# Kernel tuning notes

Hardware: AMD Instinct MI355X
Metric: run time of the kernel (lower is better)

The kernel has to match this reference:

```python
import jax, jax.numpy as jnp
import numpy as np

DIM = 1024
MAXLEN = 2048
EPS = 1e-6


def rms_norm(x, w):
    rms = jnp.sqrt(jnp.mean(x * x, axis=-1, keepdims=True) + EPS)
    return x / rms * w


def setup_inputs() -> dict:
    key = jax.random.key(0)
    ks = jax.random.split(key, 12)
    d = DIM
    s = 0.02
    inp = {
        "x": jax.random.normal(ks[0], (8, 2048, d), dtype=jnp.float32),
        "attn_norm_w": jnp.ones((d,), jnp.float32),
        "mlp_norm_w": jnp.ones((d,), jnp.float32),
        "wq": jax.random.normal(ks[1], (d, d), jnp.float32) * s,
        "bq": jnp.zeros((d,), jnp.float32),
        "wk": jax.random.normal(ks[2], (d, d), jnp.float32) * s,
        "bk": jnp.zeros((d,), jnp.float32),
        "wv": jax.random.normal(ks[3], (d, d), jnp.float32) * s,
        "bv": jnp.zeros((d,), jnp.float32),
        "wo": jax.random.normal(ks[4], (d, d), jnp.float32) * s,
        "bo": jnp.zeros((d,), jnp.float32),
        "w1": jax.random.normal(ks[5], (d, 4 * d), jnp.float32) * s,
        "b1": jnp.zeros((4 * d,), jnp.float32),
        "w2": jax.random.normal(ks[6], (4 * d, d), jnp.float32) * s,
        "b2": jnp.zeros((d,), jnp.float32),
    }
    return inp


def reference(x, attn_norm_w, mlp_norm_w, wq, bq, wk, bk, wv, bv, wo, bo, w1, b1, w2, b2):
    b, t, d = x.shape
    xn = rms_norm(x, attn_norm_w)
    q = xn @ wq + bq
    k = xn @ wk + bk
    v = xn @ wv + bv
    # single-head attention over full dim, scaled by sqrt(d)
    scores = jnp.einsum("btd,bsd->bts", q, k) / jnp.sqrt(jnp.asarray(d, x.dtype))
    causal = jnp.tril(jnp.ones((t, t), dtype=bool))
    scores = jnp.where(causal, scores, jnp.asarray(-1e9, x.dtype))
    probs = jax.nn.softmax(scores, axis=-1)
    attn = jnp.einsum("bts,bsd->btd", probs, v)
    x = x + attn @ wo + bo
    h = rms_norm(x, mlp_norm_w)
    x = x + jax.nn.gelu(h @ w1 + b1, approximate=False) @ w2 + b2
    return x
```

## Files before the change

kernel.cpp:

```cpp
#include <hip/hip_runtime.h>
#include <hip/hip_bf16.h>

typedef __bf16 bf16;
typedef __bf16 bf16x8 __attribute__((ext_vector_type(8)));
typedef __bf16 bf16x4 __attribute__((ext_vector_type(4)));
typedef float  f32x4  __attribute__((ext_vector_type(4)));

#define DIM   1024
#define SEQ   2048
#define BATCH 8
#define NROWS (BATCH * SEQ)
#define HID   4096

__device__ __forceinline__ void async_ld16(const bf16* g, bf16* l) {
    __builtin_amdgcn_global_load_lds(
        (__attribute__((address_space(1))) void*)(g),
        (__attribute__((address_space(3))) void*)(l),
        16, 0, 0);
}

__device__ __forceinline__ f32x4 mfma16(bf16x8 a, bf16x8 b, f32x4 c) {
    return __builtin_amdgcn_mfma_f32_16x16x32_bf16(a, b, c, 0, 0, 0);
}

template<int OUTF32, int BIASMODE, int RESID, int GELU, int SCORE, int PV>
__global__ __launch_bounds__(512, 2) void gemm256_kernel(
    const bf16* __restrict__ A, size_t aB,
    const bf16* __restrict__ B, size_t bB,
    void* __restrict__ Cv, size_t cB,
    const float* __restrict__ bias,
    const float* __restrict__ resid,
    int M, int N, int K, float scale)
{
    __shared__ alignas(16) bf16 LA[2 * 2 * 8192];
    __shared__ alignas(16) bf16 LB[2 * 2 * 8192];

    const int gx = gridDim.x;
    int lin = blockIdx.y * gx + blockIdx.x;
    {
        const int nwg = gx * gridDim.y;
        const int q = nwg >> 3, r = nwg & 7;
        const int xcd = lin & 7, o = lin >> 3;
        lin = (xcd < r ? xcd * (q + 1) : r * (q + 1) + (xcd - r) * q) + o;
    }
    const int m0 = (lin / gx) * 256;
    const int n0 = (lin % gx) * 256;
    if (SCORE && n0 >= m0 + 256) return;

    const int z = blockIdx.z;
    A += (size_t)z * aB;
    B += (size_t)z * bB;

    const int t    = threadIdx.x;
    const int lane = t & 63;
    const int wave = t >> 6;
    const int wr   = wave >> 2;
    const int wc   = wave & 3;

    const int kEnd = PV ? (m0 + 256) : K;
    const int NT   = kEnd >> 6;

    const int srow = t >> 3;
    const int sd   = ((t & 7) ^ (srow & 7)) * 8;
    const bf16* gA = A + (size_t)(m0 + srow) * (size_t)K + sd;
    const bf16* gB = B + (size_t)(n0 + srow) * (size_t)K + sd;
    bf16* const lA = LA + wave * 512;
    bf16* const lB = LB + wave * 512;
    const size_t rowblk = (size_t)64 * (size_t)K;

#define STG_A(db, hf, T) do {                                               \
    const bf16* g_ = gA + (size_t)((hf) * 2) * rowblk + (size_t)(T) * 64;   \
    async_ld16(g_,          lA + ((db) * 2 + (hf)) * 8192);                 \
    async_ld16(g_ + rowblk, lA + ((db) * 2 + (hf)) * 8192 + 4096);          \
} while (0)
#define STG_B(db, hf, T) do {                                               \
    const bf16* g_ = gB + (size_t)((hf) * 2) * rowblk + (size_t)(T) * 64;   \
    async_ld16(g_,          lB + ((db) * 2 + (hf)) * 8192);                 \
    async_ld16(g_ + rowblk, lB + ((db) * 2 + (hf)) * 8192 + 4096);          \
} while (0)

    const int fr    = lane & 15;
    const int fg    = lane >> 4;
    const int pc0   = ((fg)     ^ (fr & 7)) * 8;
    const int pc1   = ((4 + fg) ^ (fr & 7)) * 8;
    const int raOff = (wr * 64 + fr) * 64;
    const int rbOff = (wc * 32 + fr) * 64;

    f32x4  acc[2][2][4][2] = {};
    bf16x8 af[4][2];
    bf16x8 bg[2][2][2];

#define LDF_A(db, hf) do { _Pragma("unroll")                                  \
    for (int mi_ = 0; mi_ < 4; ++mi_) {                                       \
        const bf16* p_ = LA + ((db) * 2 + (hf)) * 8192 + raOff + mi_ * 1024;  \
        af[mi_][0] = *(const bf16x8*)(p_ + pc0);                              \
        af[mi_][1] = *(const bf16x8*)(p_ + pc1); } } while (0)
#define LDF_B(db, hf) do { _Pragma("unroll")                                  \
    for (int ni_ = 0; ni_ < 2; ++ni_) {                                       \
        const bf16* p_ = LB + ((db) * 2 + (hf)) * 8192 + rbOff + ni_ * 1024;  \
        bg[hf][ni_][0] = *(const bf16x8*)(p_ + pc0);                          \
        bg[hf][ni_][1] = *(const bf16x8*)(p_ + pc1); } } while (0)
#define MFMAQ(qm, qn) do {                                                    \
    __builtin_amdgcn_s_setprio(1);                                            \
    _Pragma("unroll") for (int mi_ = 0; mi_ < 4; ++mi_)                       \
    _Pragma("unroll") for (int ni_ = 0; ni_ < 2; ++ni_) {                     \
        acc[qm][qn][mi_][ni_] = mfma16(af[mi_][0], bg[qn][ni_][0], acc[qm][qn][mi_][ni_]); \
        acc[qm][qn][mi_][ni_] = mfma16(af[mi_][1], bg[qn][ni_][1], acc[qm][qn][mi_][ni_]); } \
    __builtin_amdgcn_s_setprio(0);                                            \
} while (0)
#define LGKM0 do { asm volatile("s_waitcnt lgkmcnt(0)" ::: "memory");         \
                   __builtin_amdgcn_sched_barrier(0); } while (0)
#define VM6   asm volatile("s_waitcnt vmcnt(6)" ::: "memory")
#define VM8   asm volatile("s_waitcnt vmcnt(8)" ::: "memory")
#define BAR   __builtin_amdgcn_s_barrier()

    STG_A(0, 0, 0); STG_B(0, 0, 0); STG_B(0, 1, 0); STG_A(0, 1, 0);
    STG_A(1, 0, 1); STG_B(1, 0, 1); STG_B(1, 1, 1); STG_A(1, 1, 1);
    VM8;
    BAR;
    LDF_A(0, 0); LDF_B(0, 0); LDF_B(0, 1);

    for (int kt = 0; kt < NT; kt += 2) {
        const int Tp2 = (kt + 2 < NT) ? kt + 2 : NT - 1;
        const int Tp3 = (kt + 3 < NT) ? kt + 3 : NT - 1;

        LGKM0;
        STG_A(0, 0, Tp2); STG_B(0, 0, Tp2);
        MFMAQ(0, 0); MFMAQ(0, 1);
        LDF_A(0, 1);
        VM6; BAR;

        LGKM0;
        STG_B(0, 1, Tp2); STG_A(0, 1, Tp2);
        MFMAQ(1, 0);
        LDF_B(1, 0);
        MFMAQ(1, 1);
        LDF_B(1, 1);
        LDF_A(1, 0);
        VM8; BAR;

        LGKM0;
        STG_A(1, 0, Tp3); STG_B(1, 0, Tp3);
        MFMAQ(0, 0); MFMAQ(0, 1);
        LDF_A(1, 1);
        VM6; BAR;

        LGKM0;
        STG_B(1, 1, Tp3); STG_A(1, 1, Tp3);
        MFMAQ(1, 0);
        LDF_B(0, 0);
        MFMAQ(1, 1);
        LDF_B(0, 1);
        LDF_A(0, 0);
        VM8; BAR;
    }

    const int col  = lane & 15;
    const int row4 = (lane >> 4) * 4;
    const size_t cOff = (size_t)z * cB;
    #pragma unroll
    for (int qm = 0; qm < 2; ++qm)
    #pragma unroll
    for (int mi = 0; mi < 4; ++mi) {
        const int mBase = m0 + qm * 128 + wr * 64 + mi * 16 + row4;
        #pragma unroll
        for (int qn = 0; qn < 2; ++qn)
        #pragma unroll
        for (int ni = 0; ni < 2; ++ni) {
            const int n = n0 + qn * 128 + wc * 32 + ni * 16 + col;
            const float bcol = (BIASMODE == 1) ? bias[n] : 0.0f;
            #pragma unroll
            for (int r = 0; r < 4; ++r) {
                const int m = mBase + r;
                float v = acc[qm][qn][mi][ni][r];
                if (BIASMODE == 1) v += bcol;
                if (BIASMODE == 2) v += bias[m];
                if (SCORE) { v *= scale; if (n > m) v = -1e30f; }
                if (GELU)  { v = 0.5f * v * (1.0f + erff(v * 0.70710678118654752f)); }
                const size_t idx = cOff + (size_t)m * (size_t)N + (size_t)n;
                if (RESID) v += resid[idx];
                if (OUTF32) ((float*)Cv)[idx] = v;
                else        ((bf16*)Cv)[idx]  = (bf16)v;
            }
        }
    }
#undef STG_A
#undef STG_B
#undef LDF_A
#undef LDF_B
#undef MFMAQ
#undef LGKM0
#undef VM6
#undef VM8
#undef BAR
}

__global__ __launch_bounds__(256) void rmsnorm_kernel(
    const float* __restrict__ x, const float* __restrict__ w, bf16* __restrict__ out)
{
    const int row = blockIdx.x;
    const int t   = threadIdx.x;
    const float4 v = ((const float4*)(x + (size_t)row * DIM))[t];
    float ss = v.x * v.x + v.y * v.y + v.z * v.z + v.w * v.w;
    #pragma unroll
    for (int off = 32; off; off >>= 1) ss += __shfl_down(ss, off);
    __shared__ float part[4];
    if ((t & 63) == 0) part[t >> 6] = ss;
    __syncthreads();
    const float tot  = part[0] + part[1] + part[2] + part[3];
    const float rinv = rsqrtf(tot * (1.0f / DIM) + 1e-6f);
    const float4 wv = ((const float4*)w)[t];
    bf16x4 o;
    o[0] = (bf16)(v.x * rinv * wv.x);
    o[1] = (bf16)(v.y * rinv * wv.y);
    o[2] = (bf16)(v.z * rinv * wv.z);
    o[3] = (bf16)(v.w * rinv * wv.w);
    *(bf16x4*)(out + (size_t)row * DIM + t * 4) = o;
}

__global__ __launch_bounds__(256) void transpose_w_kernel(
    const float* __restrict__ src, bf16* __restrict__ dst, int R, int C)
{
    __shared__ float tile[32][33];
    const int tx = threadIdx.x & 31;
    const int ty = threadIdx.x >> 5;
    const int c0 = blockIdx.x * 32;
    const int r0 = blockIdx.y * 32;
    #pragma unroll
    for (int j = 0; j < 32; j += 8)
        tile[ty + j][tx] = src[(size_t)(r0 + ty + j) * C + c0 + tx];
    __syncthreads();
    #pragma unroll
    for (int j = 0; j < 32; j += 8)
        dst[(size_t)(c0 + ty + j) * R + r0 + tx] = (bf16)tile[tx][ty + j];
}

__global__ __launch_bounds__(256) void softmax_kernel(bf16* __restrict__ S)
{
    const int t = blockIdx.x;
    const int b = blockIdx.y;
    bf16* p = S + ((size_t)b * SEQ + t) * SEQ;
    const int send = ((t >> 8) + 1) << 8;
    const int tid  = threadIdx.x;
    const int lane = tid & 63;
    const int wave = tid >> 6;

    float v[8];
    int cnt = 0;
    float m = -3.0e38f;
    for (int i = tid; i < send; i += 256) { const float f = (float)p[i]; v[cnt++] = f; m = fmaxf(m, f); }
    #pragma unroll
    for (int off = 32; off; off >>= 1) m = fmaxf(m, __shfl_down(m, off));
    __shared__ float red[4];
    if (lane == 0) red[wave] = m;
    __syncthreads();
    m = fmaxf(fmaxf(red[0], red[1]), fmaxf(red[2], red[3]));
    __syncthreads();

    float s = 0.0f;
    for (int k2 = 0; k2 < cnt; ++k2) { v[k2] = __expf(v[k2] - m); s += v[k2]; }
    #pragma unroll
    for (int off = 32; off; off >>= 1) s += __shfl_down(s, off);
    if (lane == 0) red[wave] = s;
    __syncthreads();
    s = red[0] + red[1] + red[2] + red[3];
    const float inv = 1.0f / s;
    cnt = 0;
    for (int i = tid; i < send; i += 256) p[i] = (bf16)(v[cnt++] * inv);
}

extern "C" void kernel_launch(void* const* d_in, const int* in_sizes, int n_in,
                              void* d_out, int out_size, void* d_ws, size_t ws_size,
                              hipStream_t stream)
{
    const float* x   = (const float*)d_in[0];
    const float* anw = (const float*)d_in[1];
    const float* mnw = (const float*)d_in[2];
    const float* wq  = (const float*)d_in[3];
    const float* bq  = (const float*)d_in[4];
    const float* wk  = (const float*)d_in[5];
    const float* bk  = (const float*)d_in[6];
    const float* wv  = (const float*)d_in[7];
    const float* bv  = (const float*)d_in[8];
    const float* wo  = (const float*)d_in[9];
    const float* bo  = (const float*)d_in[10];
    const float* w1  = (const float*)d_in[11];
    const float* b1  = (const float*)d_in[12];
    const float* w2  = (const float*)d_in[13];
    const float* b2  = (const float*)d_in[14];
    float* out = (float*)d_out;

    char* ws = (char*)d_ws;
    const size_t MB = 1024 * 1024;
    bf16* wqT = (bf16*)(ws + 0 * MB);
    bf16* wkT = (bf16*)(ws + 2 * MB);
    bf16* wvT = (bf16*)(ws + 4 * MB);
    bf16* woT = (bf16*)(ws + 6 * MB);
    bf16* w1T = (bf16*)(ws + 8 * MB);
    bf16* w2T = (bf16*)(ws + 16 * MB);
    bf16* xn  = (bf16*)(ws + 24 * MB);
    bf16* q   = (bf16*)(ws + 56 * MB);
    bf16* k   = (bf16*)(ws + 88 * MB);
    bf16* vT  = (bf16*)(ws + 120 * MB);
    bf16* S   = (bf16*)(ws + 152 * MB);
    bf16* attn = xn;
    bf16* h    = q;
    bf16* mid  = k;

    const dim3 blk(256);
    const dim3 blkG(512);

    transpose_w_kernel<<<dim3(DIM / 32, DIM / 32), blk, 0, stream>>>(wq, wqT, DIM, DIM);
    transpose_w_kernel<<<dim3(DIM / 32, DIM / 32), blk, 0, stream>>>(wk, wkT, DIM, DIM);
    transpose_w_kernel<<<dim3(DIM / 32, DIM / 32), blk, 0, stream>>>(wv, wvT, DIM, DIM);
    transpose_w_kernel<<<dim3(DIM / 32, DIM / 32), blk, 0, stream>>>(wo, woT, DIM, DIM);
    transpose_w_kernel<<<dim3(HID / 32, DIM / 32), blk, 0, stream>>>(w1, w1T, DIM, HID);
    transpose_w_kernel<<<dim3(DIM / 32, HID / 32), blk, 0, stream>>>(w2, w2T, HID, DIM);

    rmsnorm_kernel<<<NROWS, blk, 0, stream>>>(x, anw, xn);

    gemm256_kernel<0, 1, 0, 0, 0, 0><<<dim3(DIM / 256, NROWS / 256, 1), blkG, 0, stream>>>(
        xn, 0, wqT, 0, q, 0, bq, nullptr, NROWS, DIM, DIM, 1.0f);
    gemm256_kernel<0, 1, 0, 0, 0, 0><<<dim3(DIM / 256, NROWS / 256, 1), blkG, 0, stream>>>(
        xn, 0, wkT, 0, k, 0, bk, nullptr, NROWS, DIM, DIM, 1.0f);
    gemm256_kernel<0, 2, 0, 0, 0, 0><<<dim3(SEQ / 256, DIM / 256, BATCH), blkG, 0, stream>>>(
        wvT, 0, xn, (size_t)SEQ * DIM, vT, (size_t)DIM * SEQ, bv, nullptr, DIM, SEQ, DIM, 1.0f);

    gemm256_kernel<0, 0, 0, 0, 1, 0><<<dim3(SEQ / 256, SEQ / 256, BATCH), blkG, 0, stream>>>(
        q, (size_t)SEQ * DIM, k, (size_t)SEQ * DIM, S, (size_t)SEQ * SEQ,
        nullptr, nullptr, SEQ, SEQ, DIM, 0.03125f);

    softmax_kernel<<<dim3(SEQ, BATCH), blk, 0, stream>>>(S);

    gemm256_kernel<0, 0, 0, 0, 0, 1><<<dim3(DIM / 256, SEQ / 256, BATCH), blkG, 0, stream>>>(
        S, (size_t)SEQ * SEQ, vT, (size_t)DIM * SEQ, attn, (size_t)SEQ * DIM,
        nullptr, nullptr, SEQ, DIM, SEQ, 1.0f);

    gemm256_kernel<1, 1, 1, 0, 0, 0><<<dim3(DIM / 256, NROWS / 256, 1), blkG, 0, stream>>>(
        attn, 0, woT, 0, out, 0, bo, x, NROWS, DIM, DIM, 1.0f);

    rmsnorm_kernel<<<NROWS, blk, 0, stream>>>(out, mnw, h);

    gemm256_kernel<0, 1, 0, 1, 0, 0><<<dim3(HID / 256, NROWS / 256, 1), blkG, 0, stream>>>(
        h, 0, w1T, 0, mid, 0, b1, nullptr, NROWS, HID, DIM, 1.0f);

    gemm256_kernel<1, 1, 1, 0, 0, 0><<<dim3(DIM / 256, NROWS / 256, 1), blkG, 0, stream>>>(
        mid, 0, w2T, 0, out, 0, b2, out, NROWS, DIM, HID, 1.0f);
}
```

Before: 860.8 us.

## Fuse Q and K projections into one GEMM and drop XCD tile remapping

Merges the separate Q and K projection GEMMs into a single N=2048 GEMM that writes an interleaved qk buffer, relying on wqT and wkT sitting next to each other in the workspace. The score GEMM now reads q and k through explicit leading dimensions. This replaces one kernel launch and lets the A operand be shared across the combined tile grid. It also removes the XCD-aware block index remapping in favor of plain blockIdx mapping, which may hurt L2 locality across chiplets for every GEMM.

```diff
diff --git a/kernel.cpp b/kernel.cpp
--- a/kernel.cpp
+++ b/kernel.cpp
@@ -25,26 +25,19 @@
 
 template<int OUTF32, int BIASMODE, int RESID, int GELU, int SCORE, int PV>
 __global__ __launch_bounds__(512, 2) void gemm256_kernel(
-    const bf16* __restrict__ A, size_t aB,
-    const bf16* __restrict__ B, size_t bB,
+    const bf16* __restrict__ A, size_t aB, int lda,
+    const bf16* __restrict__ B, size_t bB, int ldb,
     void* __restrict__ Cv, size_t cB,
     const float* __restrict__ bias,
+    const float* __restrict__ bias2,
     const float* __restrict__ resid,
     int M, int N, int K, float scale)
 {
     __shared__ alignas(16) bf16 LA[2 * 2 * 8192];
     __shared__ alignas(16) bf16 LB[2 * 2 * 8192];
 
-    const int gx = gridDim.x;
-    int lin = blockIdx.y * gx + blockIdx.x;
-    {
-        const int nwg = gx * gridDim.y;
-        const int q = nwg >> 3, r = nwg & 7;
-        const int xcd = lin & 7, o = lin >> 3;
-        lin = (xcd < r ? xcd * (q + 1) : r * (q + 1) + (xcd - r) * q) + o;
-    }
-    const int m0 = (lin / gx) * 256;
-    const int n0 = (lin % gx) * 256;
+    const int m0 = blockIdx.y * 256;
+    const int n0 = blockIdx.x * 256;
     if (SCORE && n0 >= m0 + 256) return;
 
     const int z = blockIdx.z;
@@ -62,21 +55,22 @@
 
     const int srow = t >> 3;
     const int sd   = ((t & 7) ^ (srow & 7)) * 8;
-    const bf16* gA = A + (size_t)(m0 + srow) * (size_t)K + sd;
-    const bf16* gB = B + (size_t)(n0 + srow) * (size_t)K + sd;
+    const bf16* gA = A + (size_t)(m0 + srow) * (size_t)lda + sd;
+    const bf16* gB = B + (size_t)(n0 + srow) * (size_t)ldb + sd;
     bf16* const lA = LA + wave * 512;
     bf16* const lB = LB + wave * 512;
-    const size_t rowblk = (size_t)64 * (size_t)K;
+    const size_t rowA = (size_t)64 * (size_t)lda;
+    const size_t rowB = (size_t)64 * (size_t)ldb;
 
 #define STG_A(db, hf, T) do {                                               \
-    const bf16* g_ = gA + (size_t)((hf) * 2) * rowblk + (size_t)(T) * 64;   \
-    async_ld16(g_,          lA + ((db) * 2 + (hf)) * 8192);                 \
-    async_ld16(g_ + rowblk, lA + ((db) * 2 + (hf)) * 8192 + 4096);          \
+    const bf16* g_ = gA + (size_t)((hf) * 2) * rowA + (size_t)(T) * 64;     \
+    async_ld16(g_,        lA + ((db) * 2 + (hf)) * 8192);                   \
+    async_ld16(g_ + rowA, lA + ((db) * 2 + (hf)) * 8192 + 4096);            \
 } while (0)
 #define STG_B(db, hf, T) do {                                               \
-    const bf16* g_ = gB + (size_t)((hf) * 2) * rowblk + (size_t)(T) * 64;   \
-    async_ld16(g_,          lB + ((db) * 2 + (hf)) * 8192);                 \
-    async_ld16(g_ + rowblk, lB + ((db) * 2 + (hf)) * 8192 + 4096);          \
+    const bf16* g_ = gB + (size_t)((hf) * 2) * rowB + (size_t)(T) * 64;     \
+    async_ld16(g_,        lB + ((db) * 2 + (hf)) * 8192);                   \
+    async_ld16(g_ + rowB, lB + ((db) * 2 + (hf)) * 8192 + 4096);            \
 } while (0)
 
     const int fr    = lane & 15;
@@ -168,12 +162,14 @@
         #pragma unroll
         for (int ni = 0; ni < 2; ++ni) {
             const int n = n0 + qn * 128 + wc * 32 + ni * 16 + col;
-            const float bcol = (BIASMODE == 1) ? bias[n] : 0.0f;
+            float bcol = 0.0f;
+            if (BIASMODE == 1) bcol = bias[n];
+            if (BIASMODE == 3) bcol = (n < 1024) ? bias[n] : bias2[n - 1024];
             #pragma unroll
             for (int r = 0; r < 4; ++r) {
                 const int m = mBase + r;
                 float v = acc[qm][qn][mi][ni][r];
-                if (BIASMODE == 1) v += bcol;
+                if (BIASMODE == 1 || BIASMODE == 3) v += bcol;
                 if (BIASMODE == 2) v += bias[m];
                 if (SCORE) { v *= scale; if (n > m) v = -1e30f; }
                 if (GELU)  { v = 0.5f * v * (1.0f + erff(v * 0.70710678118654752f)); }
@@ -299,13 +295,12 @@
     bf16* w1T = (bf16*)(ws + 8 * MB);
     bf16* w2T = (bf16*)(ws + 16 * MB);
     bf16* xn  = (bf16*)(ws + 24 * MB);
-    bf16* q   = (bf16*)(ws + 56 * MB);
-    bf16* k   = (bf16*)(ws + 88 * MB);
+    bf16* qk  = (bf16*)(ws + 56 * MB);
     bf16* vT  = (bf16*)(ws + 120 * MB);
     bf16* S   = (bf16*)(ws + 152 * MB);
     bf16* attn = xn;
-    bf16* h    = q;
-    bf16* mid  = k;
+    bf16* h    = qk;
+    bf16* mid  = (bf16*)(ws + 88 * MB);
 
     const dim3 blk(256);
     const dim3 blkG(512);
@@ -319,31 +314,31 @@
 
     rmsnorm_kernel<<<NROWS, blk, 0, stream>>>(x, anw, xn);
 
-    gemm256_kernel<0, 1, 0, 0, 0, 0><<<dim3(DIM / 256, NROWS / 256, 1), blkG, 0, stream>>>(
-        xn, 0, wqT, 0, q, 0, bq, nullptr, NROWS, DIM, DIM, 1.0f);
-    gemm256_kernel<0, 1, 0, 0, 0, 0><<<dim3(DIM / 256, NROWS / 256, 1), blkG, 0, stream>>>(
-        xn, 0, wkT, 0, k, 0, bk, nullptr, NROWS, DIM, DIM, 1.0f);
+    gemm256_kernel<0, 3, 0, 0, 0, 0><<<dim3(2048 / 256, NROWS / 256, 1), blkG, 0, stream>>>(
+        xn, 0, DIM, wqT, 0, DIM, qk, 0, bq, bk, nullptr, NROWS, 2048, DIM, 1.0f);
+
     gemm256_kernel<0, 2, 0, 0, 0, 0><<<dim3(SEQ / 256, DIM / 256, BATCH), blkG, 0, stream>>>(
-        wvT, 0, xn, (size_t)SEQ * DIM, vT, (size_t)DIM * SEQ, bv, nullptr, DIM, SEQ, DIM, 1.0f);
+        wvT, 0, DIM, xn, (size_t)SEQ * DIM, DIM, vT, (size_t)DIM * SEQ,
+        bv, nullptr, nullptr, DIM, SEQ, DIM, 1.0f);
 
     gemm256_kernel<0, 0, 0, 0, 1, 0><<<dim3(SEQ / 256, SEQ / 256, BATCH), blkG, 0, stream>>>(
-        q, (size_t)SEQ * DIM, k, (size_t)SEQ * DIM, S, (size_t)SEQ * SEQ,
-        nullptr, nullptr, SEQ, SEQ, DIM, 0.03125f);
+        qk, (size_t)SEQ * 2048, 2048, qk + 1024, (size_t)SEQ * 2048, 2048,
+        S, (size_t)SEQ * SEQ, nullptr, nullptr, nullptr, SEQ, SEQ, DIM, 0.03125f);
 
     softmax_kernel<<<dim3(SEQ, BATCH), blk, 0, stream>>>(S);
 
     gemm256_kernel<0, 0, 0, 0, 0, 1><<<dim3(DIM / 256, SEQ / 256, BATCH), blkG, 0, stream>>>(
-        S, (size_t)SEQ * SEQ, vT, (size_t)DIM * SEQ, attn, (size_t)SEQ * DIM,
-        nullptr, nullptr, SEQ, DIM, SEQ, 1.0f);
+        S, (size_t)SEQ * SEQ, SEQ, vT, (size_t)DIM * SEQ, SEQ,
+        attn, (size_t)SEQ * DIM, nullptr, nullptr, nullptr, SEQ, DIM, SEQ, 1.0f);
 
     gemm256_kernel<1, 1, 1, 0, 0, 0><<<dim3(DIM / 256, NROWS / 256, 1), blkG, 0, stream>>>(
-        attn, 0, woT, 0, out, 0, bo, x, NROWS, DIM, DIM, 1.0f);
+        attn, 0, DIM, woT, 0, DIM, out, 0, bo, nullptr, x, NROWS, DIM, DIM, 1.0f);
 
     rmsnorm_kernel<<<NROWS, blk, 0, stream>>>(out, mnw, h);
 
     gemm256_kernel<0, 1, 0, 1, 0, 0><<<dim3(HID / 256, NROWS / 256, 1), blkG, 0, stream>>>(
-        h, 0, w1T, 0, mid, 0, b1, nullptr, NROWS, HID, DIM, 1.0f);
+        h, 0, DIM, w1T, 0, DIM, mid, 0, b1, nullptr, nullptr, NROWS, HID, DIM, 1.0f);
 
     gemm256_kernel<1, 1, 1, 0, 0, 0><<<dim3(DIM / 256, NROWS / 256, 1), blkG, 0, stream>>>(
-        mid, 0, w2T, 0, out, 0, b2, out, NROWS, DIM, HID, 1.0f);
-}
+        mid, 0, HID, w2T, 0, HID, out, 0, b2, nullptr, out, NROWS, DIM, HID, 1.0f);
+}
```

Result: faster. 810.9 us (-5.8%).
